# Kernel optimization log

Measured on AMD Instinct MI355X. Metric: run time of the kernel, lower is better.

## Reference

```python
import jax, jax.numpy as jnp
import numpy as np

N_EMBED = 512
HEAD = 64
N_HEADS = N_EMBED // HEAD  # 8
N_LAYERS = 6
BLOCK = 2048
B = 4
T = 2048
SCALE = N_LAYERS / 3 ** (-0.25)  # = n_layers * 3**0.25, applied to q,k,v and FFN output


def setup_inputs() -> dict:
    key = jax.random.key(0)
    ks = jax.random.split(key, 8)
    sd = 1.0 / np.sqrt(N_EMBED)
    return {
        "x": jax.random.normal(ks[0], (B, T, N_EMBED), jnp.float32),
        "wq": jax.random.normal(ks[1], (N_HEADS, N_EMBED, HEAD), jnp.float32) * sd,
        "wk": jax.random.normal(ks[2], (N_HEADS, N_EMBED, HEAD), jnp.float32) * sd,
        "wv": jax.random.normal(ks[3], (N_HEADS, N_EMBED, HEAD), jnp.float32) * sd,
        "w_proj": jax.random.normal(ks[4], (N_EMBED, N_EMBED), jnp.float32) * sd,
        "b_proj": jnp.zeros((N_EMBED,), jnp.float32),
        "w1": jax.random.normal(ks[5], (N_EMBED, 4 * N_EMBED), jnp.float32) * sd,
        "b1": jnp.zeros((4 * N_EMBED,), jnp.float32),
        "w2": jax.random.normal(ks[6], (4 * N_EMBED, N_EMBED), jnp.float32) / np.sqrt(4 * N_EMBED),
        "b2": jnp.zeros((N_EMBED,), jnp.float32),
        "g1": jnp.ones((N_EMBED,), jnp.float32),
        "be1": jnp.zeros((N_EMBED,), jnp.float32),
        "g2": jnp.ones((N_EMBED,), jnp.float32),
        "be2": jnp.zeros((N_EMBED,), jnp.float32),
    }


def _layernorm(x, g, b, eps=1e-5):
    mu = jnp.mean(x, axis=-1, keepdims=True)
    var = jnp.var(x, axis=-1, keepdims=True)
    return (x - mu) * jax.lax.rsqrt(var + eps) * g + b


def _attention(x, wq, wk, wv, w_proj, b_proj):
    # x: [B,T,C]; wq/wk/wv: [H,C,D]  (vectorized over the per-head Linears)
    q = jnp.einsum("btc,hcd->bhtd", x, wq) * SCALE
    k = jnp.einsum("btc,hcd->bhtd", x, wk) * SCALE
    v = jnp.einsum("btc,hcd->bhtd", x, wv) * SCALE
    # NOTE: original scales by C**-0.5 where C = n_embed (input dim), not head_size
    wei = jnp.einsum("bhtd,bhsd->bhts", q, k) * (N_EMBED ** -0.5)
    causal = jnp.tril(jnp.ones((T, T), bool))  # tril buffer, sliced to [T,T]
    wei = jnp.where(causal, wei, -jnp.inf)
    wei = jax.nn.softmax(wei, axis=-1)
    out = jnp.einsum("bhts,bhsd->bhtd", wei, v)
    out = out.transpose(0, 2, 1, 3).reshape(x.shape)  # concat heads on last dim
    return out @ w_proj + b_proj


def _feedforward(x, w1, b1, w2, b2):
    h = jax.nn.relu(x @ w1 + b1)
    return (h @ w2 + b2) * SCALE


def reference(x, wq, wk, wv, w_proj, b_proj, w1, b1, w2, b2, g1, be1, g2, be2):
    x = x + _attention(_layernorm(x, g1, be1), wq, wk, wv, w_proj, b_proj)
    x = x + _feedforward(_layernorm(x, g2, be2), w1, b1, w2, b2)
    return x
```

## Files before the change

kernel.cpp:

```cpp
#include <hip/hip_runtime.h>

typedef _Float16 f16;
typedef f16 f16x4 __attribute__((ext_vector_type(4)));
typedef f16 f16x8 __attribute__((ext_vector_type(8)));
typedef float f32x4 __attribute__((ext_vector_type(4)));

#define AS1 __attribute__((address_space(1)))
#define AS3 __attribute__((address_space(3)))

constexpr float kScale  = 7.896444077714954f;
constexpr float kScaleQ = (float)(7.896444077714954 / 22.627416997969522 * 1.4426950408889634);

__device__ __forceinline__ void g2l16(const void* g, void* l) {
  __builtin_amdgcn_global_load_lds((const AS1 void*)g, (AS3 void*)l, 16, 0, 0);
}

__global__ __launch_bounds__(256) void ln_kernel(
    const float* __restrict__ x, const float* __restrict__ g,
    const float* __restrict__ be, f16* __restrict__ out) {
  int row = blockIdx.x * 4 + (threadIdx.x >> 6);
  int lane = threadIdx.x & 63;
  const float* xr = x + (size_t)row * 512;
  float xa[8];
  *(float4*)&xa[0] = *(const float4*)(xr + lane * 8);
  *(float4*)&xa[4] = *(const float4*)(xr + lane * 8 + 4);
  float s = 0.f, q = 0.f;
#pragma unroll
  for (int i = 0; i < 8; ++i) { s += xa[i]; q += xa[i] * xa[i]; }
#pragma unroll
  for (int off = 32; off; off >>= 1) { s += __shfl_xor(s, off); q += __shfl_xor(q, off); }
  float mean = s * (1.f / 512.f);
  float var = q * (1.f / 512.f) - mean * mean;
  float rstd = rsqrtf(var + 1e-5f);
  float ga[8], ba[8];
  *(float4*)&ga[0] = *(const float4*)(g + lane * 8);
  *(float4*)&ga[4] = *(const float4*)(g + lane * 8 + 4);
  *(float4*)&ba[0] = *(const float4*)(be + lane * 8);
  *(float4*)&ba[4] = *(const float4*)(be + lane * 8 + 4);
  f16x8 o;
#pragma unroll
  for (int i = 0; i < 8; ++i) o[i] = (f16)((xa[i] - mean) * rstd * ga[i] + ba[i]);
  *(f16x8*)(out + (size_t)row * 512 + lane * 8) = o;
}

__global__ __launch_bounds__(256) void transpose_cvt(
    const float* __restrict__ in, f16* __restrict__ out,
    int R, int Cc, long ibs, long obs, float scale) {
  __shared__ float t[32][33];
  int b = blockIdx.z;
  const float* im = in + (size_t)b * ibs;
  int c0 = blockIdx.x * 32, r0 = blockIdx.y * 32;
  int tx = threadIdx.x & 31, ty = threadIdx.x >> 5;
#pragma unroll
  for (int i = 0; i < 4; ++i) {
    int rr = ty + i * 8;
    t[rr][tx] = im[(size_t)(r0 + rr) * Cc + c0 + tx] * scale;
  }
  __syncthreads();
#pragma unroll
  for (int i = 0; i < 4; ++i) {
    int rr = ty + i * 8;
    out[(size_t)b * obs + (size_t)(c0 + rr) * R + r0 + tx] = (f16)t[tx][rr];
  }
}

template <int MODE, bool W8>
__global__ __launch_bounds__(W8 ? 512 : 256) void gemm_bt(
    const f16* __restrict__ A, const f16* __restrict__ Bt,
    const float* __restrict__ bias, const float* __restrict__ res,
    float* __restrict__ outf, f16* __restrict__ outb,
    f16* __restrict__ qo, f16* __restrict__ ko, f16* __restrict__ vo,
    int N, int K) {
  __shared__ f16 lA[2][128 * 64], lB[2][128 * 64];
  constexpr int NF = W8 ? 2 : 4;
  constexpr int WCW = W8 ? 32 : 64;
  int tid = threadIdx.x;
  int lane = tid & 63, w = tid >> 6;
  int wr = W8 ? (w >> 2) : (w >> 1);
  int wc = W8 ? (w & 3) : (w & 1);
  int gq = lane >> 4, r = lane & 15;
  int m0 = blockIdx.x * 128, n0 = blockIdx.y * 128;
  size_t Kb = (size_t)K * 2;
  const char* Ab = (const char*)A + (size_t)m0 * Kb;
  const char* Bb = (const char*)Bt + (size_t)n0 * Kb;
  f32x4 acc[4][NF] = {};
  int srow = lane >> 3, sslot = lane & 7;
  auto stage = [&](int buf, int kt) {
#pragma unroll
    for (int i = 0; i < (W8 ? 2 : 4); ++i) {
      int chunk = i * (W8 ? 8 : 4) + w;
      int row = chunk * 8 + srow;
      int slot = sslot ^ (row & 7);
      g2l16(Ab + (size_t)row * Kb + kt * 2 + slot * 16, (char*)lA + buf * 16384 + chunk * 1024);
      g2l16(Bb + (size_t)row * Kb + kt * 2 + slot * 16, (char*)lB + buf * 16384 + chunk * 1024);
    }
  };
  stage(0, 0);
  int cur = 0;
  for (int kt = 0; kt < K; kt += 64) {
    __syncthreads();
    if (kt + 64 < K) stage(cur ^ 1, kt + 64);
    const char* bA = (const char*)lA + cur * 16384;
    const char* bB = (const char*)lB + cur * 16384;
    f16x8 af[4][2], bfr[NF][2];
#pragma unroll
    for (int f = 0; f < 4; ++f)
#pragma unroll
      for (int ks = 0; ks < 2; ++ks) {
        int ra = wr * 64 + f * 16 + r;
        af[f][ks] = *(const f16x8*)(bA + ra * 128 + (((ks * 4 + gq) ^ (ra & 7)) * 16));
      }
#pragma unroll
    for (int fn = 0; fn < NF; ++fn)
#pragma unroll
      for (int ks = 0; ks < 2; ++ks) {
        int rb = wc * WCW + fn * 16 + r;
        bfr[fn][ks] = *(const f16x8*)(bB + rb * 128 + (((ks * 4 + gq) ^ (rb & 7)) * 16));
      }
    __builtin_amdgcn_s_setprio(1);
#pragma unroll
    for (int fm = 0; fm < 4; ++fm)
#pragma unroll
      for (int fn = 0; fn < NF; ++fn)
#pragma unroll
        for (int ks = 0; ks < 2; ++ks)
          acc[fm][fn] = __builtin_amdgcn_mfma_f32_16x16x32_f16(af[fm][ks], bfr[fn][ks], acc[fm][fn], 0, 0, 0);
    __builtin_amdgcn_s_setprio(0);
    cur ^= 1;
  }
#pragma unroll
  for (int fm = 0; fm < 4; ++fm)
#pragma unroll
    for (int fn = 0; fn < NF; ++fn)
#pragma unroll
      for (int rg = 0; rg < 4; ++rg) {
        int row = m0 + wr * 64 + fm * 16 + gq * 4 + rg;
        int col = n0 + wc * WCW + fn * 16 + r;
        float v = acc[fm][fn][rg];
        if constexpr (MODE == 1) {
          outf[(size_t)row * N + col] = v + bias[col] + res[(size_t)row * N + col];
        } else if constexpr (MODE == 2) {
          outb[(size_t)row * N + col] = (f16)fmaxf(v + bias[col], 0.f);
        } else if constexpr (MODE == 3) {
          outf[(size_t)row * N + col] = v + bias[col] * kScale + res[(size_t)row * N + col];
        } else {
          int bb = row >> 11, t = row & 2047;
          int which = col >> 9, hd = col & 511, hh = hd >> 6, d = hd & 63;
          size_t bh = (size_t)bb * 8 + hh;
          if (which == 0)      qo[(bh * 2048 + t) * 64 + d] = (f16)v;
          else if (which == 1) ko[(bh * 2048 + t) * 64 + d] = (f16)v;
          else                 vo[(bh * 64 + d) * 2048 + t] = (f16)v;
        }
      }
}

__global__ __launch_bounds__(256) void attn_kernel(
    const f16* __restrict__ Q, const f16* __restrict__ K,
    const f16* __restrict__ Vt, f16* __restrict__ out) {
  __shared__ f16 lK[2][64 * 64], lV[2][64 * 64];
  __shared__ f16 lP[4][16 * 72];
  int tid = threadIdx.x, lane = tid & 63, w = tid >> 6;
  int gq = lane >> 4, r = lane & 15;
  int bh = blockIdx.x;
  int p = blockIdx.y;
  const char* Qb = (const char*)(Q + (size_t)bh * 2048 * 64);
  const char* Kb = (const char*)(K + (size_t)bh * 2048 * 64);
  const char* Vb = (const char*)(Vt + (size_t)bh * 64 * 2048);
  int q0A = p * 64 + w * 16;
  int q0B = (31 - p) * 64 + w * 16;
  f16x8 qfA[2], qfB[2];
#pragma unroll
  for (int ks = 0; ks < 2; ++ks) {
    qfA[ks] = *(const f16x8*)(Qb + (size_t)(q0A + r) * 128 + ks * 64 + gq * 16);
    qfB[ks] = *(const f16x8*)(Qb + (size_t)(q0B + r) * 128 + ks * 64 + gq * 16);
  }
  f32x4 OA[4] = {}, OB[4] = {};
  float mA = -1e30f, lA_ = 0.f, mB = -1e30f, lB_ = 0.f;
  int srow = lane >> 3, sslot = lane & 7;

  auto stage = [&](int buf, int kv) {
    int j0 = kv * 64;
#pragma unroll
    for (int i = 0; i < 2; ++i) {
      int chunk = i * 4 + w;
      int row = chunk * 8 + srow;
      int slot = sslot ^ (row & 7);
      g2l16(Kb + (size_t)(j0 + row) * 128 + slot * 16, (char*)lK + buf * 8192 + chunk * 1024);
      g2l16(Vb + (size_t)row * 4096 + j0 * 2 + slot * 16, (char*)lV + buf * 8192 + chunk * 1024);
    }
  };

  f16x8 vf[4][2];
  auto smpv = [&](f32x4 (&s)[4], float& m, float& l, f32x4 (&O)[4]) {
    float t0 = fmaxf(fmaxf(s[0][0], s[0][1]), fmaxf(s[0][2], s[0][3]));
    float t1 = fmaxf(fmaxf(s[1][0], s[1][1]), fmaxf(s[1][2], s[1][3]));
    float t2 = fmaxf(fmaxf(s[2][0], s[2][1]), fmaxf(s[2][2], s[2][3]));
    float t3 = fmaxf(fmaxf(s[3][0], s[3][1]), fmaxf(s[3][2], s[3][3]));
    float pmax = fmaxf(fmaxf(t0, t1), fmaxf(t2, t3));
    pmax = fmaxf(pmax, __shfl_xor(pmax, 16));
    pmax = fmaxf(pmax, __shfl_xor(pmax, 32));
    float mn = fmaxf(m, pmax);
    if (mn - m > 11.5f) {
      float sc = exp2f(m - mn);
      l *= sc;
#pragma unroll
      for (int fd = 0; fd < 4; ++fd) O[fd] *= sc;
      m = mn;
    } else {
      mn = m;
    }
    float ps = 0.f;
#pragma unroll
    for (int fc = 0; fc < 4; ++fc) {
      f16x4 pv;
#pragma unroll
      for (int rg = 0; rg < 4; ++rg) {
        float pe = exp2f(s[fc][rg] - mn);
        ps += pe;
        pv[rg] = (f16)pe;
      }
      *(f16x4*)((char*)&lP[w][0] + r * 144 + fc * 32 + gq * 8) = pv;
    }
    ps += __shfl_xor(ps, 16);
    ps += __shfl_xor(ps, 32);
    l += ps;
    f16x8 pf[2];
#pragma unroll
    for (int ks = 0; ks < 2; ++ks)
      pf[ks] = *(const f16x8*)((const char*)&lP[w][0] + r * 144 + ks * 64 + gq * 16);
#pragma unroll
    for (int fd = 0; fd < 4; ++fd)
#pragma unroll
      for (int ks = 0; ks < 2; ++ks)
        O[fd] = __builtin_amdgcn_mfma_f32_16x16x32_f16(vf[fd][ks], pf[ks], O[fd], 0, 0, 0);
  };

  int nkv = 32 - p;
  stage(0, 0);
  int cur = 0;
  for (int kv = 0; kv < nkv; ++kv) {
    int j0 = kv * 64;
    __syncthreads();
    if (kv + 1 < nkv) stage(cur ^ 1, kv + 1);
    const char* bK = (const char*)lK + cur * 8192;
    const char* bV = (const char*)lV + cur * 8192;
    f16x8 kf[4][2];
#pragma unroll
    for (int fc = 0; fc < 4; ++fc)
#pragma unroll
      for (int ks = 0; ks < 2; ++ks) {
        int rj = fc * 16 + r;
        kf[fc][ks] = *(const f16x8*)(bK + rj * 128 + (((ks * 4 + gq) ^ (rj & 7)) * 16));
      }
#pragma unroll
    for (int fd = 0; fd < 4; ++fd)
#pragma unroll
      for (int ks = 0; ks < 2; ++ks) {
        int rd = fd * 16 + r;
        vf[fd][ks] = *(const f16x8*)(bV + rd * 128 + (((ks * 4 + gq) ^ (rd & 7)) * 16));
      }
    f32x4 sB[4] = {};
#pragma unroll
    for (int ks = 0; ks < 2; ++ks)
#pragma unroll
      for (int fc = 0; fc < 4; ++fc)
        sB[fc] = __builtin_amdgcn_mfma_f32_16x16x32_f16(kf[fc][ks], qfB[ks], sB[fc], 0, 0, 0);
    if (kv == nkv - 1) {
      int t = q0B + r;
#pragma unroll
      for (int fc = 0; fc < 4; ++fc)
#pragma unroll
        for (int rg = 0; rg < 4; ++rg) {
          int j = j0 + fc * 16 + gq * 4 + rg;
          if (j > t) sB[fc][rg] = -1e30f;
        }
    }
    smpv(sB, mB, lB_, OB);
    if (kv <= p) {
      f32x4 sA[4] = {};
#pragma unroll
      for (int ks = 0; ks < 2; ++ks)
#pragma unroll
        for (int fc = 0; fc < 4; ++fc)
          sA[fc] = __builtin_amdgcn_mfma_f32_16x16x32_f16(kf[fc][ks], qfA[ks], sA[fc], 0, 0, 0);
      if (kv == p) {
        int t = q0A + r;
#pragma unroll
        for (int fc = 0; fc < 4; ++fc)
#pragma unroll
          for (int rg = 0; rg < 4; ++rg) {
            int j = j0 + fc * 16 + gq * 4 + rg;
            if (j > t) sA[fc][rg] = -1e30f;
          }
      }
      smpv(sA, mA, lA_, OA);
    }
    cur ^= 1;
  }
  int bb = bh >> 3, hh = bh & 7;
  auto wout = [&](int q0, f32x4 (&O)[4], float l) {
    float inv = 1.f / l;
    int t = q0 + r;
    f16* o = out + ((size_t)bb * 2048 + t) * 512 + hh * 64 + gq * 4;
#pragma unroll
    for (int fd = 0; fd < 4; ++fd) {
      f16x4 v;
#pragma unroll
      for (int rg = 0; rg < 4; ++rg) v[rg] = (f16)(O[fd][rg] * inv);
      *(f16x4*)(o + fd * 16) = v;
    }
  };
  wout(q0A, OA, lA_);
  wout(q0B, OB, lB_);
}

extern "C" void kernel_launch(void* const* d_in, const int* in_sizes, int n_in,
                              void* d_out, int out_size, void* d_ws, size_t ws_size,
                              hipStream_t stream) {
  (void)in_sizes; (void)n_in; (void)out_size; (void)ws_size;
  const float* x      = (const float*)d_in[0];
  const float* wq     = (const float*)d_in[1];
  const float* wk     = (const float*)d_in[2];
  const float* wv     = (const float*)d_in[3];
  const float* w_proj = (const float*)d_in[4];
  const float* b_proj = (const float*)d_in[5];
  const float* w1     = (const float*)d_in[6];
  const float* b1     = (const float*)d_in[7];
  const float* w2     = (const float*)d_in[8];
  const float* b2     = (const float*)d_in[9];
  const float* g1     = (const float*)d_in[10];
  const float* be1    = (const float*)d_in[11];
  const float* g2     = (const float*)d_in[12];
  const float* be2    = (const float*)d_in[13];
  float* outp = (float*)d_out;

  char* ws = (char*)d_ws;
  size_t off = 0;
  auto alloc = [&](size_t bytes) {
    char* p = ws + off;
    off += (bytes + 255) & ~(size_t)255;
    return p;
  };
  const size_t MC2 = (size_t)8192 * 512 * 2;
  f16* x_ln  = (f16*)alloc(MC2);
  f16* qb    = (f16*)alloc(MC2);
  f16* kb    = (f16*)alloc(MC2);
  f16* vb    = (f16*)alloc(MC2);
  f16* attn  = (f16*)alloc(MC2);
  float* x1  = (float*)alloc((size_t)8192 * 512 * 4);
  f16* Wqkv  = (f16*)alloc((size_t)1536 * 512 * 2);
  f16* Wp    = (f16*)alloc((size_t)512 * 512 * 2);
  f16* W1t   = (f16*)alloc((size_t)2048 * 512 * 2);
  f16* W2t   = (f16*)alloc((size_t)512 * 2048 * 2);
  f16* x1_ln = x_ln;
  f16* hbuf  = qb;

  transpose_cvt<<<dim3(2, 16, 8), 256, 0, stream>>>(wq, Wqkv,                 512, 64, 512 * 64, 64 * 512, kScaleQ);
  transpose_cvt<<<dim3(2, 16, 8), 256, 0, stream>>>(wk, Wqkv + 512 * 512,     512, 64, 512 * 64, 64 * 512, kScale);
  transpose_cvt<<<dim3(2, 16, 8), 256, 0, stream>>>(wv, Wqkv + 2 * 512 * 512, 512, 64, 512 * 64, 64 * 512, kScale);
  transpose_cvt<<<dim3(16, 16, 1), 256, 0, stream>>>(w_proj, Wp, 512, 512, 0, 0, 1.f);
  transpose_cvt<<<dim3(64, 16, 1), 256, 0, stream>>>(w1, W1t, 512, 2048, 0, 0, 1.f);
  transpose_cvt<<<dim3(16, 64, 1), 256, 0, stream>>>(w2, W2t, 2048, 512, 0, 0, kScale);

  ln_kernel<<<2048, 256, 0, stream>>>(x, g1, be1, x_ln);
  gemm_bt<0, false><<<dim3(64, 12), 256, 0, stream>>>(x_ln, Wqkv, nullptr, nullptr, nullptr, nullptr,
                                                      qb, kb, vb, 1536, 512);
  attn_kernel<<<dim3(32, 16), 256, 0, stream>>>(qb, kb, vb, attn);
  gemm_bt<1, true><<<dim3(64, 4), 512, 0, stream>>>(attn, Wp, b_proj, x, x1, nullptr,
                                                    nullptr, nullptr, nullptr, 512, 512);
  ln_kernel<<<2048, 256, 0, stream>>>(x1, g2, be2, x1_ln);
  gemm_bt<2, false><<<dim3(64, 16), 256, 0, stream>>>(x1_ln, W1t, b1, nullptr, nullptr, hbuf,
                                                      nullptr, nullptr, nullptr, 2048, 512);
  gemm_bt<3, true><<<dim3(64, 4), 512, 0, stream>>>(hbuf, W2t, b2, x1, outp, nullptr,
                                                    nullptr, nullptr, nullptr, 512, 2048);
}
```

Baseline: 179.8 us.

## Fuse weight preprocessing and first layernorm into one launch; MFMA row-sum in attention

Merges the six weight transpose/convert launches and the first layernorm launch into a single preprocessing kernel that dispatches on block index. This removes six kernel launch gaps. In attention, the softmax denominator is no longer built from a scalar sum plus cross-lane shuffles. It is computed by an extra MFMA against a vector of ones, which costs two more MFMAs per tile but drops the VALU adds and shuffles. The denominator now accumulates from the f16-rounded probabilities, which slightly changes the numerics.

```diff
diff --git a/kernel.cpp b/kernel.cpp
--- a/kernel.cpp
+++ b/kernel.cpp
@@ -15,10 +15,10 @@
   __builtin_amdgcn_global_load_lds((const AS1 void*)g, (AS3 void*)l, 16, 0, 0);
 }
 
-__global__ __launch_bounds__(256) void ln_kernel(
+__device__ __forceinline__ void ln_body(
     const float* __restrict__ x, const float* __restrict__ g,
-    const float* __restrict__ be, f16* __restrict__ out) {
-  int row = blockIdx.x * 4 + (threadIdx.x >> 6);
+    const float* __restrict__ be, f16* __restrict__ out, int rowblk) {
+  int row = rowblk * 4 + ((int)threadIdx.x >> 6);
   int lane = threadIdx.x & 63;
   const float* xr = x + (size_t)row * 512;
   float xa[8];
@@ -43,13 +43,43 @@
   *(f16x8*)(out + (size_t)row * 512 + lane * 8) = o;
 }
 
-__global__ __launch_bounds__(256) void transpose_cvt(
-    const float* __restrict__ in, f16* __restrict__ out,
-    int R, int Cc, long ibs, long obs, float scale) {
+__global__ __launch_bounds__(256) void ln_kernel(
+    const float* __restrict__ x, const float* __restrict__ g,
+    const float* __restrict__ be, f16* __restrict__ out) {
+  ln_body(x, g, be, out, blockIdx.x);
+}
+
+__global__ __launch_bounds__(256) void preproc_kernel(
+    const float* __restrict__ wq, const float* __restrict__ wk,
+    const float* __restrict__ wv, const float* __restrict__ wp,
+    const float* __restrict__ w1, const float* __restrict__ w2,
+    const float* __restrict__ x, const float* __restrict__ g1,
+    const float* __restrict__ be1,
+    f16* __restrict__ Wqkv, f16* __restrict__ Wp, f16* __restrict__ W1t,
+    f16* __restrict__ W2t, f16* __restrict__ x_ln) {
+  int bid = blockIdx.x;
+  if (bid >= 3072) { ln_body(x, g1, be1, x_ln, bid - 3072); return; }
   __shared__ float t[32][33];
-  int b = blockIdx.z;
-  const float* im = in + (size_t)b * ibs;
-  int c0 = blockIdx.x * 32, r0 = blockIdx.y * 32;
+  const float* in; f16* out; int R, Cc, bx, by, bz = 0; float scale;
+  if (bid < 768) {
+    int which = bid >> 8, rem = bid & 255;
+    bx = rem & 1; by = (rem >> 1) & 15; bz = rem >> 5;
+    in = which == 0 ? wq : (which == 1 ? wk : wv);
+    out = Wqkv + (size_t)which * 512 * 512;
+    R = 512; Cc = 64; scale = which == 0 ? kScaleQ : kScale;
+  } else if (bid < 1024) {
+    int rem = bid - 768; bx = rem & 15; by = rem >> 4;
+    in = wp; out = Wp; R = 512; Cc = 512; scale = 1.f;
+  } else if (bid < 2048) {
+    int rem = bid - 1024; bx = rem & 63; by = rem >> 6;
+    in = w1; out = W1t; R = 512; Cc = 2048; scale = 1.f;
+  } else {
+    int rem = bid - 2048; bx = rem & 15; by = rem >> 4;
+    in = w2; out = W2t; R = 2048; Cc = 512; scale = kScale;
+  }
+  const float* im = in + (size_t)bz * R * Cc;
+  f16* om = out + (size_t)bz * Cc * R;
+  int c0 = bx * 32, r0 = by * 32;
   int tx = threadIdx.x & 31, ty = threadIdx.x >> 5;
 #pragma unroll
   for (int i = 0; i < 4; ++i) {
@@ -60,7 +90,7 @@
 #pragma unroll
   for (int i = 0; i < 4; ++i) {
     int rr = ty + i * 8;
-    out[(size_t)b * obs + (size_t)(c0 + rr) * R + r0 + tx] = (f16)t[tx][rr];
+    om[(size_t)(c0 + rr) * R + r0 + tx] = (f16)t[tx][rr];
   }
 }
 
@@ -174,8 +204,11 @@
     qfA[ks] = *(const f16x8*)(Qb + (size_t)(q0A + r) * 128 + ks * 64 + gq * 16);
     qfB[ks] = *(const f16x8*)(Qb + (size_t)(q0B + r) * 128 + ks * 64 + gq * 16);
   }
-  f32x4 OA[4] = {}, OB[4] = {};
-  float mA = -1e30f, lA_ = 0.f, mB = -1e30f, lB_ = 0.f;
+  f16x8 ones;
+#pragma unroll
+  for (int i = 0; i < 8; ++i) ones[i] = (f16)1.f;
+  f32x4 OA[4] = {}, OB[4] = {}, OlA = {}, OlB = {};
+  float mA = -1e30f, mB = -1e30f;
   int srow = lane >> 3, sslot = lane & 7;
 
   auto stage = [&](int buf, int kv) {
@@ -191,7 +224,7 @@
   };
 
   f16x8 vf[4][2];
-  auto smpv = [&](f32x4 (&s)[4], float& m, float& l, f32x4 (&O)[4]) {
+  auto smpv = [&](f32x4 (&s)[4], float& m, f32x4 (&O)[4], f32x4& Ol) {
     float t0 = fmaxf(fmaxf(s[0][0], s[0][1]), fmaxf(s[0][2], s[0][3]));
     float t1 = fmaxf(fmaxf(s[1][0], s[1][1]), fmaxf(s[1][2], s[1][3]));
     float t2 = fmaxf(fmaxf(s[2][0], s[2][1]), fmaxf(s[2][2], s[2][3]));
@@ -202,28 +235,20 @@
     float mn = fmaxf(m, pmax);
     if (mn - m > 11.5f) {
       float sc = exp2f(m - mn);
-      l *= sc;
 #pragma unroll
       for (int fd = 0; fd < 4; ++fd) O[fd] *= sc;
+      Ol *= sc;
       m = mn;
     } else {
       mn = m;
     }
-    float ps = 0.f;
 #pragma unroll
     for (int fc = 0; fc < 4; ++fc) {
       f16x4 pv;
 #pragma unroll
-      for (int rg = 0; rg < 4; ++rg) {
-        float pe = exp2f(s[fc][rg] - mn);
-        ps += pe;
-        pv[rg] = (f16)pe;
-      }
+      for (int rg = 0; rg < 4; ++rg) pv[rg] = (f16)exp2f(s[fc][rg] - mn);
       *(f16x4*)((char*)&lP[w][0] + r * 144 + fc * 32 + gq * 8) = pv;
     }
-    ps += __shfl_xor(ps, 16);
-    ps += __shfl_xor(ps, 32);
-    l += ps;
     f16x8 pf[2];
 #pragma unroll
     for (int ks = 0; ks < 2; ++ks)
@@ -233,6 +258,9 @@
 #pragma unroll
       for (int ks = 0; ks < 2; ++ks)
         O[fd] = __builtin_amdgcn_mfma_f32_16x16x32_f16(vf[fd][ks], pf[ks], O[fd], 0, 0, 0);
+#pragma unroll
+    for (int ks = 0; ks < 2; ++ks)
+      Ol = __builtin_amdgcn_mfma_f32_16x16x32_f16(ones, pf[ks], Ol, 0, 0, 0);
   };
 
   int nkv = 32 - p;
@@ -275,7 +303,7 @@
           if (j > t) sB[fc][rg] = -1e30f;
         }
     }
-    smpv(sB, mB, lB_, OB);
+    smpv(sB, mB, OB, OlB);
     if (kv <= p) {
       f32x4 sA[4] = {};
 #pragma unroll
@@ -293,7 +321,7 @@
             if (j > t) sA[fc][rg] = -1e30f;
           }
       }
-      smpv(sA, mA, lA_, OA);
+      smpv(sA, mA, OA, OlA);
     }
     cur ^= 1;
   }
@@ -310,8 +338,8 @@
       *(f16x4*)(o + fd * 16) = v;
     }
   };
-  wout(q0A, OA, lA_);
-  wout(q0B, OB, lB_);
+  wout(q0A, OA, OlA[0]);
+  wout(q0B, OB, OlB[0]);
 }
 
 extern "C" void kernel_launch(void* const* d_in, const int* in_sizes, int n_in,
@@ -355,14 +383,8 @@
   f16* x1_ln = x_ln;
   f16* hbuf  = qb;
 
-  transpose_cvt<<<dim3(2, 16, 8), 256, 0, stream>>>(wq, Wqkv,                 512, 64, 512 * 64, 64 * 512, kScaleQ);
-  transpose_cvt<<<dim3(2, 16, 8), 256, 0, stream>>>(wk, Wqkv + 512 * 512,     512, 64, 512 * 64, 64 * 512, kScale);
-  transpose_cvt<<<dim3(2, 16, 8), 256, 0, stream>>>(wv, Wqkv + 2 * 512 * 512, 512, 64, 512 * 64, 64 * 512, kScale);
-  transpose_cvt<<<dim3(16, 16, 1), 256, 0, stream>>>(w_proj, Wp, 512, 512, 0, 0, 1.f);
-  transpose_cvt<<<dim3(64, 16, 1), 256, 0, stream>>>(w1, W1t, 512, 2048, 0, 0, 1.f);
-  transpose_cvt<<<dim3(16, 64, 1), 256, 0, stream>>>(w2, W2t, 2048, 512, 0, 0, kScale);
-
-  ln_kernel<<<2048, 256, 0, stream>>>(x, g1, be1, x_ln);
+  preproc_kernel<<<5120, 256, 0, stream>>>(wq, wk, wv, w_proj, w1, w2, x, g1, be1,
+                                           Wqkv, Wp, W1t, W2t, x_ln);
   gemm_bt<0, false><<<dim3(64, 12), 256, 0, stream>>>(x_ln, Wqkv, nullptr, nullptr, nullptr, nullptr,
                                                       qb, kb, vb, 1536, 512);
   attn_kernel<<<dim3(32, 16), 256, 0, stream>>>(qb, kb, vb, attn);
```

After: 165.9 us. 7.7% less time.
